# Performance work log

Measured on AMD Instinct MI355X. Metric: run time of the kernel, lower is better.

The kernel has to match this reference:

```python
import jax, jax.numpy as jnp
import numpy as np

N = 50000          # nodes (multiple of p+e=8)
E = 400000         # edges (avg degree 8)
H, C = 4, 128      # heads, per-head channels
IN = 5             # input node feature dim
HID = 512          # mlp hidden dim
P, EV = 4, 4       # pursuers / evaders per graph
NEG_SLOPE = 0.2    # GATConv leaky_relu slope

# static team index: nodes with idx % (P+EV) < P  (team='pursuer')
_idx = np.arange(N)
TEAM_IDX = jnp.asarray(_idx[_idx % (P + EV) < P])  # [N/2]


def setup_inputs() -> dict:
    key = jax.random.key(0)
    ks = jax.random.split(key, 16)
    s = 0.1
    return {
        "x": jax.random.normal(ks[0], (N, IN), jnp.float32),
        "edge_index": jax.random.randint(ks[1], (2, E), 0, N, jnp.int64),
        "edge_attr": jax.random.normal(ks[2], (E, 2), jnp.float32),
        # GATConv params
        "W": jax.random.normal(ks[3], (H * C, IN), jnp.float32) * s,
        "att_src": jax.random.normal(ks[4], (H, C), jnp.float32) * s,
        "att_dst": jax.random.normal(ks[5], (H, C), jnp.float32) * s,
        "bias": jnp.zeros((H * C,), jnp.float32),
        # MLP head params
        "W1": jax.random.normal(ks[6], (HID, H * C), jnp.float32) * s,
        "b1": jnp.zeros((HID,), jnp.float32),
        "W2": jax.random.normal(ks[7], (HID, HID), jnp.float32) * s,
        "b2": jnp.zeros((HID,), jnp.float32),
        "W3": jax.random.normal(ks[8], (2, HID), jnp.float32) * s,
        "b3": jnp.zeros((2,), jnp.float32),
    }


def _gat_max(x, src, dst, W, att_src, att_dst, bias):
    # linear transform: [N, H, C]
    h = (x @ W.T).reshape(N, H, C)
    a_src = jnp.einsum("nhc,hc->nh", h, att_src)  # [N, H]
    a_dst = jnp.einsum("nhc,hc->nh", h, att_dst)  # [N, H]
    # per-edge attention logits, leaky relu
    alpha = jax.nn.leaky_relu(a_src[src] + a_dst[dst], NEG_SLOPE)  # [Et, H]
    # segment softmax over incoming edges of each dst node
    amax = jax.ops.segment_max(alpha, dst, num_segments=N)  # [N, H]
    ex = jnp.exp(alpha - amax[dst])
    den = jax.ops.segment_sum(ex, dst, num_segments=N)      # [N, H]
    attn = ex / den[dst]                                     # [Et, H]
    # alpha-weighted messages, scatter-MAX aggregation (aggr='max')
    msg = h[src] * attn[:, :, None]                          # [Et, H, C]
    out = jax.ops.segment_max(msg, dst, num_segments=N)     # [N, H, C]
    return out.reshape(N, H * C) + bias


def reference(x, edge_index, edge_attr, W, att_src, att_dst, bias,
              W1, b1, W2, b2, W3, b3):
    # PyG GATConv default add_self_loops=True; edge_attr ignored (edge_dim=None)
    loops = jnp.arange(N, dtype=edge_index.dtype)
    src = jnp.concatenate([edge_index[0], loops])
    dst = jnp.concatenate([edge_index[1], loops])
    emb = _gat_max(x, src, dst, W, att_src, att_dst, bias)  # [N, 512]
    h = emb[TEAM_IDX]                                        # [N/2, 512]
    h = jax.nn.relu(h @ W1.T + b1)
    h = jax.nn.relu(h @ W2.T + b2)
    return jnp.tanh(h @ W3.T + b3)                           # [N/2, 2]
```

## Files before the change

### kernel.cpp

```cpp
#include <hip/hip_runtime.h>
#include <hip/hip_bf16.h>
#include <math.h>

#define N_NODES 50000
#define N_EDGES 400000
#define HEADS   4
#define HC      512
#define IN_DIM  5
#define M_SEL   25000
#define NEG_SLOPE 0.2f

typedef __attribute__((ext_vector_type(8))) short bf16x8;
typedef __attribute__((ext_vector_type(4))) float f32x4;

__device__ inline unsigned short f2bf(float f) {
    union { float f; unsigned u; } v; v.f = f;
    unsigned r = v.u + 0x7FFF + ((v.u >> 16) & 1);
    return (unsigned short)(r >> 16);
}
__device__ inline float bf2f(unsigned short b) {
    union { unsigned u; float f; } v; v.u = ((unsigned)b) << 16;
    return v.f;
}

#define TR_NPW 8

__global__ __launch_bounds__(256) void k_transform(
        const float* __restrict__ x, const float* __restrict__ W,
        const float* __restrict__ att_src, const float* __restrict__ att_dst,
        unsigned short* __restrict__ h, float* __restrict__ a_src,
        float* __restrict__ a_dst, int* __restrict__ deg) {
    int wave = threadIdx.x >> 6, lane = threadIdx.x & 63;
    int c0 = lane * 8;

    float wreg[40];
    const float4* wp = (const float4*)(W + c0 * IN_DIM);
#pragma unroll
    for (int i = 0; i < 10; i++) ((float4*)wreg)[i] = wp[i];
    float sas[8], sad[8];
    *(float4*)&sas[0] = *(const float4*)(att_src + c0);
    *(float4*)&sas[4] = *(const float4*)(att_src + c0 + 4);
    *(float4*)&sad[0] = *(const float4*)(att_dst + c0);
    *(float4*)&sad[4] = *(const float4*)(att_dst + c0 + 4);

    int n0 = (blockIdx.x * 4 + wave) * TR_NPW;
#pragma unroll
    for (int t = 0; t < TR_NPW; t++) {
        int n = n0 + t;
        if (n >= N_NODES) return;
        float xv[IN_DIM];
#pragma unroll
        for (int i = 0; i < IN_DIM; i++) xv[i] = x[n * IN_DIM + i];

        float ps = 0.f, pd = 0.f;
        bf16x8 hv8;
#pragma unroll
        for (int j = 0; j < 8; j++) {
            float acc = 0.f;
#pragma unroll
            for (int i = 0; i < IN_DIM; i++) acc += xv[i] * wreg[j * IN_DIM + i];
            hv8[j] = (short)f2bf(acc);
            ps += acc * sas[j];
            pd += acc * sad[j];
        }
        *(bf16x8*)(h + (size_t)n * HC + c0) = hv8;

#pragma unroll
        for (int off = 8; off >= 1; off >>= 1) {
            ps += __shfl_xor(ps, off);
            pd += __shfl_xor(pd, off);
        }
        if ((lane & 15) == 0) {
            int head = lane >> 4;
            a_src[n * HEADS + head] = ps;
            a_dst[n * HEADS + head] = pd;
        }
        if (lane == 0) deg[n] = 1;
    }
}

__global__ void k_hist(const int* __restrict__ ei, int* __restrict__ deg) {
    int e = blockIdx.x * 256 + threadIdx.x;
    if (e < N_EDGES) atomicAdd(&deg[ei[N_EDGES + e]], 1);
}

#define NSCAN_BLK 196

__global__ void k_scan1(const int* __restrict__ deg, int* __restrict__ excl,
                        int* __restrict__ bsum) {
    __shared__ int s[256];
    int i = blockIdx.x * 256 + threadIdx.x;
    int v = (i < N_NODES) ? deg[i] : 0;
    s[threadIdx.x] = v;
    __syncthreads();
    for (int off = 1; off < 256; off <<= 1) {
        int t = (threadIdx.x >= off) ? s[threadIdx.x - off] : 0;
        __syncthreads();
        s[threadIdx.x] += t;
        __syncthreads();
    }
    if (i < N_NODES) excl[i] = s[threadIdx.x] - v;
    if (threadIdx.x == 255) bsum[blockIdx.x] = s[255];
}

__global__ void k_scan3fill(const int* __restrict__ excl, const int* __restrict__ bsum,
                            int* __restrict__ offs, int* __restrict__ curs,
                            int* __restrict__ csr) {
    __shared__ int part[256];
    int tid = threadIdx.x;
    part[tid] = (tid < NSCAN_BLK) ? bsum[tid] : 0;
    __syncthreads();
    for (int off = 1; off < 256; off <<= 1) {
        int t = (tid >= off) ? part[tid - off] : 0;
        __syncthreads();
        part[tid] += t;
        __syncthreads();
    }
    int blockoff = (blockIdx.x == 0) ? 0 : part[blockIdx.x - 1];
    int i = blockIdx.x * 256 + tid;
    if (i < N_NODES) {
        int o = excl[i] + blockoff;
        offs[i] = o;
        csr[o] = i;
        curs[i] = o + 1;
    }
}

__global__ void k_fill_edges(const int* __restrict__ ei, int* __restrict__ cursor,
                             int* __restrict__ csr) {
    int e = blockIdx.x * 256 + threadIdx.x;
    if (e < N_EDGES) {
        int d = ei[N_EDGES + e];
        int pos = atomicAdd(&cursor[d], 1);
        csr[pos] = ei[e];
    }
}

__global__ void k_aggregate(const unsigned short* __restrict__ h, const float* __restrict__ a_src,
                            const float* __restrict__ a_dst, const int* __restrict__ csr,
                            const int* __restrict__ offs, const int* __restrict__ deg,
                            const float* __restrict__ bias, unsigned short* __restrict__ emb_sel) {
    int wave = threadIdx.x >> 6, lane = threadIdx.x & 63;
    int w = blockIdx.x * 4 + wave;
    if (w >= M_SEL) return;
    int n = ((w >> 2) << 3) + (w & 3);

    int base = offs[n];
    int dn = deg[n];
    int head = lane >> 4, egrp = lane & 15;
    int c0 = lane * 8;

    float acc[8];
#pragma unroll
    for (int j = 0; j < 8; j++) acc[j] = -INFINITY;

    if (dn <= 16) {
        int s_e = 0;
        if (egrp < dn) s_e = csr[base + egrp];

        bf16x8 v[16];
#pragma unroll
        for (int e = 0; e < 16; e++) {
            if (e < dn) {
                int s = __shfl(s_e, e);
                v[e] = *(const bf16x8*)(h + (size_t)s * HC + c0);
            }
        }

        float adn = a_dst[n * HEADS + head];
        float t = -INFINITY;
        if (egrp < dn) {
            t = a_src[s_e * HEADS + head] + adn;
            t = (t > 0.f) ? t : NEG_SLOPE * t;
        }
        float m = t;
#pragma unroll
        for (int off = 8; off >= 1; off >>= 1) m = fmaxf(m, __shfl_xor(m, off));
        float ex = (egrp < dn) ? __expf(t - m) : 0.f;
        float den = ex;
#pragma unroll
        for (int off = 8; off >= 1; off >>= 1) den += __shfl_xor(den, off);
        float attn = ex / den;

#pragma unroll
        for (int e = 0; e < 16; e++) {
            if (e < dn) {
                float a = __shfl(attn, (head << 4) | e);
#pragma unroll
                for (int j = 0; j < 8; j++)
                    acc[j] = fmaxf(acc[j], bf2f((unsigned short)v[e][j]) * a);
            }
        }
    } else {
        float adn = a_dst[n * HEADS + head];
        float m = -INFINITY;
        for (int e0 = 0; e0 < dn; e0 += 16) {
            int e = e0 + egrp;
            if (e < dn) {
                int s = csr[base + e];
                float t = a_src[s * HEADS + head] + adn;
                t = (t > 0.f) ? t : NEG_SLOPE * t;
                m = fmaxf(m, t);
            }
        }
#pragma unroll
        for (int off = 8; off >= 1; off >>= 1) m = fmaxf(m, __shfl_xor(m, off));
        float den = 0.f;
        for (int e0 = 0; e0 < dn; e0 += 16) {
            int e = e0 + egrp;
            if (e < dn) {
                int s = csr[base + e];
                float t = a_src[s * HEADS + head] + adn;
                t = (t > 0.f) ? t : NEG_SLOPE * t;
                den += __expf(t - m);
            }
        }
#pragma unroll
        for (int off = 8; off >= 1; off >>= 1) den += __shfl_xor(den, off);
        float invden = 1.0f / den;
        for (int e = 0; e < dn; e++) {
            int s = csr[base + e];
            float t = a_src[s * HEADS + head] + adn;
            t = (t > 0.f) ? t : NEG_SLOPE * t;
            float attn = __expf(t - m) * invden;
            bf16x8 hv = *(const bf16x8*)(h + (size_t)s * HC + c0);
#pragma unroll
            for (int j = 0; j < 8; j++)
                acc[j] = fmaxf(acc[j], bf2f((unsigned short)hv[j]) * attn);
        }
    }

    bf16x8 ov;
#pragma unroll
    for (int j = 0; j < 8; j++) ov[j] = (short)f2bf(acc[j] + bias[c0 + j]);
    *(bf16x8*)(emb_sel + (size_t)w * HC + c0) = ov;
}

#define BK  64
#define LDK 72

__device__ inline bf16x8 cvt8(float4 a, float4 b) {
    bf16x8 r;
    r[0] = (short)f2bf(a.x); r[1] = (short)f2bf(a.y);
    r[2] = (short)f2bf(a.z); r[3] = (short)f2bf(a.w);
    r[4] = (short)f2bf(b.x); r[5] = (short)f2bf(b.y);
    r[6] = (short)f2bf(b.z); r[7] = (short)f2bf(b.w);
    return r;
}

template <bool RELU>
__global__ __launch_bounds__(512, 2) void k_gemm(const unsigned short* __restrict__ A, int M,
                                                 const float* __restrict__ Wt,
                                                 const float* __restrict__ bias,
                                                 unsigned short* __restrict__ C) {
    __shared__ unsigned short As[256 * LDK];
    __shared__ unsigned short Bs[256 * LDK];
    int tid = threadIdx.x;
    int m0 = blockIdx.y * 256;
    int o0 = blockIdx.x * 256;
    int wv = tid >> 6, lane = tid & 63;
    int wm = wv >> 1, wn = wv & 1;

    f32x4 acc[4][8];
#pragma unroll
    for (int i = 0; i < 4; i++)
#pragma unroll
        for (int j = 0; j < 8; j++) acc[i][j] = (f32x4){0.f, 0.f, 0.f, 0.f};

    bf16x8 ra[4], rb[4];
#pragma unroll
    for (int s = 0; s < 4; s++) {
        int c = s * 512 + tid;
        int row = c >> 3, col = (c & 7) * 8;
        int m = m0 + row;
        bf16x8 av = {0, 0, 0, 0, 0, 0, 0, 0};
        if (m < M) av = *(const bf16x8*)(A + (size_t)m * HC + col);
        ra[s] = av;
        const float4* wp = (const float4*)(Wt + (size_t)(o0 + row) * HC + col);
        rb[s] = cvt8(wp[0], wp[1]);
    }

    for (int k0 = 0; k0 < HC; k0 += BK) {
        __syncthreads();
#pragma unroll
        for (int s = 0; s < 4; s++) {
            int c = s * 512 + tid;
            int row = c >> 3, col = (c & 7) * 8;
            *(bf16x8*)(&As[row * LDK + col]) = ra[s];
            *(bf16x8*)(&Bs[row * LDK + col]) = rb[s];
        }
        __syncthreads();

        int kn = k0 + BK;
        if (kn < HC) {
#pragma unroll
            for (int s = 0; s < 4; s++) {
                int c = s * 512 + tid;
                int row = c >> 3, col = (c & 7) * 8;
                int m = m0 + row;
                bf16x8 av = {0, 0, 0, 0, 0, 0, 0, 0};
                if (m < M) av = *(const bf16x8*)(A + (size_t)m * HC + kn + col);
                ra[s] = av;
                const float4* wp = (const float4*)(Wt + (size_t)(o0 + row) * HC + kn + col);
                rb[s] = cvt8(wp[0], wp[1]);
            }
        }

#pragma unroll
        for (int kk = 0; kk < 2; kk++) {
            int kb = kk * 32 + (lane >> 4) * 8;
            bf16x8 af[4], bfr[8];
#pragma unroll
            for (int mi = 0; mi < 4; mi++)
                af[mi] = *(const bf16x8*)(&As[(wm * 64 + mi * 16 + (lane & 15)) * LDK + kb]);
#pragma unroll
            for (int ni = 0; ni < 8; ni++)
                bfr[ni] = *(const bf16x8*)(&Bs[(wn * 128 + ni * 16 + (lane & 15)) * LDK + kb]);
#pragma unroll
            for (int mi = 0; mi < 4; mi++)
#pragma unroll
                for (int ni = 0; ni < 8; ni++)
                    acc[mi][ni] = __builtin_amdgcn_mfma_f32_16x16x32_bf16(
                        af[mi], bfr[ni], acc[mi][ni], 0, 0, 0);
        }
    }

#pragma unroll
    for (int ni = 0; ni < 8; ni++) {
        int ncol = o0 + wn * 128 + ni * 16 + (lane & 15);
        float bv = bias[ncol];
#pragma unroll
        for (int mi = 0; mi < 4; mi++) {
            int mbase = m0 + wm * 64 + mi * 16 + (lane >> 4) * 4;
#pragma unroll
            for (int r = 0; r < 4; r++) {
                int m = mbase + r;
                if (m < M) {
                    float v = acc[mi][ni][r] + bv;
                    if (RELU) v = fmaxf(v, 0.f);
                    C[(size_t)m * HC + ncol] = f2bf(v);
                }
            }
        }
    }
}

__global__ void k_final(const unsigned short* __restrict__ h2, const float* __restrict__ W3,
                        const float* __restrict__ b3, float* __restrict__ out, int M) {
    int wave = threadIdx.x >> 6, lane = threadIdx.x & 63;
    int m = blockIdx.x * 4 + wave;
    if (m >= M) return;
    float s0 = 0.f, s1 = 0.f;
    bf16x8 hv = *(const bf16x8*)(h2 + (size_t)m * HC + lane * 8);
#pragma unroll
    for (int j = 0; j < 8; j++) {
        int k = lane * 8 + j;
        float v = bf2f((unsigned short)hv[j]);
        s0 += v * W3[k];
        s1 += v * W3[HC + k];
    }
#pragma unroll
    for (int off = 32; off >= 1; off >>= 1) {
        s0 += __shfl_xor(s0, off);
        s1 += __shfl_xor(s1, off);
    }
    if (lane == 0) {
        out[(size_t)m * 2 + 0] = tanhf(s0 + b3[0]);
        out[(size_t)m * 2 + 1] = tanhf(s1 + b3[1]);
    }
}

extern "C" void kernel_launch(void* const* d_in, const int* in_sizes, int n_in,
                              void* d_out, int out_size, void* d_ws, size_t ws_size,
                              hipStream_t stream) {
    const float* x       = (const float*)d_in[0];
    const int*   ei      = (const int*)d_in[1];
    const float* W       = (const float*)d_in[3];
    const float* att_src = (const float*)d_in[4];
    const float* att_dst = (const float*)d_in[5];
    const float* bias    = (const float*)d_in[6];
    const float* W1      = (const float*)d_in[7];
    const float* b1      = (const float*)d_in[8];
    const float* W2      = (const float*)d_in[9];
    const float* b2      = (const float*)d_in[10];
    const float* W3      = (const float*)d_in[11];
    const float* b3      = (const float*)d_in[12];
    float* out = (float*)d_out;

    char* ws = (char*)d_ws;
    unsigned short* h       = (unsigned short*)(ws);
    unsigned short* emb_sel = (unsigned short*)(ws + 51200000);
    unsigned short* h1      = (unsigned short*)(ws + 76800000);
    unsigned short* h2      = (unsigned short*)(ws + 102400000);
    float* a_src = (float*)(ws + 129048576);
    float* a_dst = (float*)(ws + 129848576);
    int*   deg   = (int*)  (ws + 130648576);
    int*   offs  = (int*)  (ws + 130848576);
    int*   curs  = (int*)  (ws + 131048576);
    int*   excl  = (int*)  (ws + 131248576);
    int*   bsum  = (int*)  (ws + 131448576);
    int*   csr   = (int*)  (ws + 131449600);

    k_transform<<<(N_NODES + 31) / 32, 256, 0, stream>>>(x, W, att_src, att_dst, h,
                                                         a_src, a_dst, deg);
    k_hist<<<(N_EDGES + 255) / 256, 256, 0, stream>>>(ei, deg);
    k_scan1<<<NSCAN_BLK, 256, 0, stream>>>(deg, excl, bsum);
    k_scan3fill<<<NSCAN_BLK, 256, 0, stream>>>(excl, bsum, offs, curs, csr);
    k_fill_edges<<<(N_EDGES + 255) / 256, 256, 0, stream>>>(ei, curs, csr);
    k_aggregate<<<6250, 256, 0, stream>>>(h, a_src, a_dst, csr, offs, deg, bias, emb_sel);

    dim3 g(2, 98);
    k_gemm<true><<<g, 512, 0, stream>>>(emb_sel, M_SEL, W1, b1, h1);
    k_gemm<true><<<g, 512, 0, stream>>>(h1, M_SEL, W2, b2, h2);
    k_final<<<(M_SEL + 3) / 4, 256, 0, stream>>>(h2, W3, b3, out, M_SEL);
}
```

Baseline: 208.8 us.

## Fuse final projection into second GEMM epilogue and hoist aggregate loads

The second MLP GEMM no longer writes h2. Its epilogue applies ReLU, dots each row with W3, reduces across lanes and atomically adds partial sums into a zeroed buffer. A small tanh kernel then finishes the output. This removes a 25 MB bf16 write and reread and the separate final kernel, at the cost of float atomics, a memset and nondeterministic summation order. The aggregate kernel also gets launch bounds and issues its attention-score loads before the gather, with a sched barrier.

Result: faster. 191.7 us (-8.2%).

```diff
diff --git a/kernel.cpp b/kernel.cpp
--- a/kernel.cpp
+++ b/kernel.cpp
@@ -136,10 +136,11 @@
     }
 }
 
-__global__ void k_aggregate(const unsigned short* __restrict__ h, const float* __restrict__ a_src,
-                            const float* __restrict__ a_dst, const int* __restrict__ csr,
-                            const int* __restrict__ offs, const int* __restrict__ deg,
-                            const float* __restrict__ bias, unsigned short* __restrict__ emb_sel) {
+__global__ __launch_bounds__(256, 4) void k_aggregate(
+        const unsigned short* __restrict__ h, const float* __restrict__ a_src,
+        const float* __restrict__ a_dst, const int* __restrict__ csr,
+        const int* __restrict__ offs, const int* __restrict__ deg,
+        const float* __restrict__ bias, unsigned short* __restrict__ emb_sel) {
     int wave = threadIdx.x >> 6, lane = threadIdx.x & 63;
     int w = blockIdx.x * 4 + wave;
     if (w >= M_SEL) return;
@@ -157,6 +158,9 @@
     if (dn <= 16) {
         int s_e = 0;
         if (egrp < dn) s_e = csr[base + egrp];
+        float adn = a_dst[n * HEADS + head];
+        float araw = 0.f;
+        if (egrp < dn) araw = a_src[s_e * HEADS + head];
 
         bf16x8 v[16];
 #pragma unroll
@@ -166,11 +170,11 @@
                 v[e] = *(const bf16x8*)(h + (size_t)s * HC + c0);
             }
         }
-
-        float adn = a_dst[n * HEADS + head];
+        __builtin_amdgcn_sched_barrier(0);
+
         float t = -INFINITY;
         if (egrp < dn) {
-            t = a_src[s_e * HEADS + head] + adn;
+            t = araw + adn;
             t = (t > 0.f) ? t : NEG_SLOPE * t;
         }
         float m = t;
@@ -248,11 +252,13 @@
     return r;
 }
 
-template <bool RELU>
+template <int MODE>
 __global__ __launch_bounds__(512, 2) void k_gemm(const unsigned short* __restrict__ A, int M,
                                                  const float* __restrict__ Wt,
                                                  const float* __restrict__ bias,
-                                                 unsigned short* __restrict__ C) {
+                                                 unsigned short* __restrict__ C,
+                                                 const float* __restrict__ W3,
+                                                 float* __restrict__ part) {
     __shared__ unsigned short As[256 * LDK];
     __shared__ unsigned short Bs[256 * LDK];
     int tid = threadIdx.x;
@@ -325,49 +331,67 @@
         }
     }
 
-#pragma unroll
-    for (int ni = 0; ni < 8; ni++) {
-        int ncol = o0 + wn * 128 + ni * 16 + (lane & 15);
-        float bv = bias[ncol];
-#pragma unroll
-        for (int mi = 0; mi < 4; mi++) {
-            int mbase = m0 + wm * 64 + mi * 16 + (lane >> 4) * 4;
+    if (MODE == 0) {
+#pragma unroll
+        for (int ni = 0; ni < 8; ni++) {
+            int ncol = o0 + wn * 128 + ni * 16 + (lane & 15);
+            float bv = bias[ncol];
+#pragma unroll
+            for (int mi = 0; mi < 4; mi++) {
+                int mbase = m0 + wm * 64 + mi * 16 + (lane >> 4) * 4;
+#pragma unroll
+                for (int r = 0; r < 4; r++) {
+                    int m = mbase + r;
+                    if (m < M) {
+                        float v = fmaxf(acc[mi][ni][r] + bv, 0.f);
+                        C[(size_t)m * HC + ncol] = f2bf(v);
+                    }
+                }
+            }
+        }
+    } else {
+        float p0[4][4], p1[4][4];
+#pragma unroll
+        for (int mi = 0; mi < 4; mi++)
+#pragma unroll
+            for (int r = 0; r < 4; r++) { p0[mi][r] = 0.f; p1[mi][r] = 0.f; }
+#pragma unroll
+        for (int ni = 0; ni < 8; ni++) {
+            int ncol = o0 + wn * 128 + ni * 16 + (lane & 15);
+            float bv = bias[ncol];
+            float w0 = W3[ncol], w1 = W3[HC + ncol];
+#pragma unroll
+            for (int mi = 0; mi < 4; mi++)
+#pragma unroll
+                for (int r = 0; r < 4; r++) {
+                    float v = fmaxf(acc[mi][ni][r] + bv, 0.f);
+                    p0[mi][r] += v * w0;
+                    p1[mi][r] += v * w1;
+                }
+        }
+#pragma unroll
+        for (int mi = 0; mi < 4; mi++)
 #pragma unroll
             for (int r = 0; r < 4; r++) {
-                int m = mbase + r;
-                if (m < M) {
-                    float v = acc[mi][ni][r] + bv;
-                    if (RELU) v = fmaxf(v, 0.f);
-                    C[(size_t)m * HC + ncol] = f2bf(v);
+                float a0 = p0[mi][r], a1 = p1[mi][r];
+#pragma unroll
+                for (int off = 8; off >= 1; off >>= 1) {
+                    a0 += __shfl_xor(a0, off);
+                    a1 += __shfl_xor(a1, off);
                 }
-            }
-        }
-    }
-}
-
-__global__ void k_final(const unsigned short* __restrict__ h2, const float* __restrict__ W3,
-                        const float* __restrict__ b3, float* __restrict__ out, int M) {
-    int wave = threadIdx.x >> 6, lane = threadIdx.x & 63;
-    int m = blockIdx.x * 4 + wave;
-    if (m >= M) return;
-    float s0 = 0.f, s1 = 0.f;
-    bf16x8 hv = *(const bf16x8*)(h2 + (size_t)m * HC + lane * 8);
-#pragma unroll
-    for (int j = 0; j < 8; j++) {
-        int k = lane * 8 + j;
-        float v = bf2f((unsigned short)hv[j]);
-        s0 += v * W3[k];
-        s1 += v * W3[HC + k];
-    }
-#pragma unroll
-    for (int off = 32; off >= 1; off >>= 1) {
-        s0 += __shfl_xor(s0, off);
-        s1 += __shfl_xor(s1, off);
-    }
-    if (lane == 0) {
-        out[(size_t)m * 2 + 0] = tanhf(s0 + b3[0]);
-        out[(size_t)m * 2 + 1] = tanhf(s1 + b3[1]);
-    }
+                int m = m0 + wm * 64 + mi * 16 + (lane >> 4) * 4 + r;
+                if ((lane & 15) == 0 && m < M) {
+                    atomicAdd(&part[m * 2 + 0], a0);
+                    atomicAdd(&part[m * 2 + 1], a1);
+                }
+            }
+    }
+}
+
+__global__ void k_tanh(const float* __restrict__ part, const float* __restrict__ b3,
+                       float* __restrict__ out) {
+    int i = blockIdx.x * 256 + threadIdx.x;
+    if (i < 2 * M_SEL) out[i] = tanhf(part[i] + b3[i & 1]);
 }
 
 extern "C" void kernel_launch(void* const* d_in, const int* in_sizes, int n_in,
@@ -391,7 +415,7 @@
     unsigned short* h       = (unsigned short*)(ws);
     unsigned short* emb_sel = (unsigned short*)(ws + 51200000);
     unsigned short* h1      = (unsigned short*)(ws + 76800000);
-    unsigned short* h2      = (unsigned short*)(ws + 102400000);
+    float* part  = (float*)(ws + 102400000);
     float* a_src = (float*)(ws + 129048576);
     float* a_dst = (float*)(ws + 129848576);
     int*   deg   = (int*)  (ws + 130648576);
@@ -401,6 +425,7 @@
     int*   bsum  = (int*)  (ws + 131448576);
     int*   csr   = (int*)  (ws + 131449600);
 
+    hipMemsetAsync(part, 0, 2 * M_SEL * sizeof(float), stream);
     k_transform<<<(N_NODES + 31) / 32, 256, 0, stream>>>(x, W, att_src, att_dst, h,
                                                          a_src, a_dst, deg);
     k_hist<<<(N_EDGES + 255) / 256, 256, 0, stream>>>(ei, deg);
@@ -410,7 +435,7 @@
     k_aggregate<<<6250, 256, 0, stream>>>(h, a_src, a_dst, csr, offs, deg, bias, emb_sel);
 
     dim3 g(2, 98);
-    k_gemm<true><<<g, 512, 0, stream>>>(emb_sel, M_SEL, W1, b1, h1);
-    k_gemm<true><<<g, 512, 0, stream>>>(h1, M_SEL, W2, b2, h2);
-    k_final<<<(M_SEL + 3) / 4, 256, 0, stream>>>(h2, W3, b3, out, M_SEL);
-}
+    k_gemm<0><<<g, 512, 0, stream>>>(emb_sel, M_SEL, W1, b1, h1, nullptr, nullptr);
+    k_gemm<1><<<g, 512, 0, stream>>>(h1, M_SEL, W2, b2, nullptr, W3, part);
+    k_tanh<<<196, 256, 0, stream>>>(part, b3, out);
+}
```
